# Performance work log

Measured on AMD Instinct MI355X. Metric: run time of the kernel, lower is better.

The kernel has to match this reference:

```python
import jax, jax.numpy as jnp
import numpy as np

DIM = 1024
HEADS = 16
HEAD_DIM = DIM // HEADS


def apply_rope(x):
    # x: (B, S, H, D)
    B, S, H, D = x.shape
    half = D // 2
    freqs = 1.0 / (10000.0 ** (jnp.arange(half, dtype=jnp.float32) / half))
    pos = jnp.arange(S, dtype=jnp.float32)
    angles = pos[:, None] * freqs[None, :]          # (S, half)
    sin = jnp.sin(angles)[None, :, None, :]
    cos = jnp.cos(angles)[None, :, None, :]
    x1, x2 = x[..., :half], x[..., half:]
    return jnp.concatenate([x1 * cos - x2 * sin, x1 * sin + x2 * cos], axis=-1)


def setup_inputs() -> dict:
    key = jax.random.key(0)
    ks = jax.random.split(key, 5)
    x = jax.random.normal(ks[0], (2, 2048, DIM), dtype=jnp.float32)
    s = 1.0 / np.sqrt(DIM)
    qkv_w = jax.random.uniform(ks[1], (3 * DIM, DIM), minval=-s, maxval=s, dtype=jnp.float32)
    qkv_b = jax.random.uniform(ks[2], (3 * DIM,), minval=-s, maxval=s, dtype=jnp.float32)
    proj_w = jax.random.uniform(ks[3], (DIM, DIM), minval=-s, maxval=s, dtype=jnp.float32)
    proj_b = jax.random.uniform(ks[4], (DIM,), minval=-s, maxval=s, dtype=jnp.float32)
    return {"x": x, "qkv_w": qkv_w, "qkv_b": qkv_b, "proj_w": proj_w, "proj_b": proj_b}


def reference(x, qkv_w, qkv_b, proj_w, proj_b):
    B, S, D = x.shape
    qkv = x @ qkv_w.T + qkv_b                       # (B, S, 3D)
    q, k, v = jnp.split(qkv, 3, axis=-1)
    q = q.reshape(B, S, HEADS, HEAD_DIM)
    k = k.reshape(B, S, HEADS, HEAD_DIM)
    v = v.reshape(B, S, HEADS, HEAD_DIM)
    q = apply_rope(q)
    k = apply_rope(k)
    scale = 1.0 / np.sqrt(HEAD_DIM)
    attn = jnp.einsum('bqhd,bkhd->bhqk', q, k) * scale
    mask = jnp.triu(jnp.ones((S, S), dtype=bool), k=1)
    attn = jnp.where(mask[None, None], -1e9, attn)
    attn = jax.nn.softmax(attn, axis=-1)
    out = jnp.einsum('bhqk,bkhd->bqhd', attn, v).reshape(B, S, D)
    return out @ proj_w.T + proj_b
```

## Files before the change

### kernel.cpp

```cpp
#include <hip/hip_runtime.h>
#include <hip/hip_bf16.h>
#include <stdint.h>

typedef unsigned short u16;
typedef __attribute__((ext_vector_type(8))) short bf16x8;
typedef __attribute__((ext_vector_type(4))) float f32x4;
typedef __attribute__((ext_vector_type(16))) float f32x16;

typedef __attribute__((address_space(1))) const void gas_t;
typedef __attribute__((address_space(3))) void las_t;

#define DEV __device__ __forceinline__

DEV float bf2f(u16 v){ union{uint32_t u; float f;} x; x.u = ((uint32_t)v)<<16; return x.f; }
DEV u16 f2bf(float f){ union{float f; uint32_t u;} x; x.f=f; uint32_t r = x.u + 0x7fff + ((x.u>>16)&1u); return (u16)(r>>16); }

DEV uint32_t pk2(float a, float b){
  return (uint32_t)f2bf(a) | ((uint32_t)f2bf(b)<<16);
}

DEV uint32_t cvtpk(float a, float b){
  uint32_t r;
  asm("v_cvt_pk_bf16_f32 %0, %1, %2" : "=v"(r) : "v"(a), "v"(b));
  return r;
}

DEV void xswap(uint32_t a, uint32_t b, int hi, uint32_t& ra, uint32_t& rb){
#if __has_builtin(__builtin_amdgcn_permlane32_swap)
  auto r = __builtin_amdgcn_permlane32_swap((int)a, (int)b, false, false);
  ra = (uint32_t)r[0]; rb = (uint32_t)r[1];
#else
  uint32_t sa = (uint32_t)__shfl_xor((int)a, 32);
  uint32_t sb = (uint32_t)__shfl_xor((int)b, 32);
  ra = hi ? sb : a;
  rb = hi ? b  : sa;
#endif
}

DEV void gload_lds16(const u16* g, u16* l){
  __builtin_amdgcn_global_load_lds((gas_t*)g, (las_t*)l, 16, 0, 0);
}

__global__ void cvt_f32_bf16(const float* __restrict__ src, u16* __restrict__ dst, int n4){
  int i = blockIdx.x*blockDim.x + threadIdx.x;
  if(i < n4){
    float4 v = ((const float4*)src)[i];
    ushort4 o; o.x=f2bf(v.x); o.y=f2bf(v.y); o.z=f2bf(v.z); o.w=f2bf(v.w);
    ((ushort4*)dst)[i] = o;
  }
}

template<int OUT_F32>
__global__ __launch_bounds__(256,3)
void gemm_bt(const u16* __restrict__ A, const u16* __restrict__ Bw,
             const float* __restrict__ bias, void* __restrict__ Cp, int N)
{
  constexpr int BK = 32, KSTEPS = 1024/BK;
  __shared__ __align__(16) u16 As[3][128][BK];
  __shared__ __align__(16) u16 Bs[3][128][BK];
  const int tid = threadIdx.x, w = tid>>6, l = tid&63;
  const int a = l&15, g = l>>4;
  const int m0 = blockIdx.y*128, n0 = blockIdx.x*128;
  const int wr = w>>1, wc = w&1;
  f32x4 zero = {0.f,0.f,0.f,0.f};
  f32x4 acc[4][4];
  #pragma unroll
  for(int m=0;m<4;m++) for(int n=0;n<4;n++) acc[m][n]=zero;

  const int srow = l>>2, scol = (l&3)*8;
  const u16* Ag = A  + (size_t)(m0 + w*32 + srow)*1024 + scol;
  const u16* Bg = Bw + (size_t)(n0 + w*32 + srow)*1024 + scol;

#define STAGE(KIDX, BUF) {                                        \
    u16* ab = &As[BUF][w*32][0];                                  \
    u16* bb = &Bs[BUF][w*32][0];                                  \
    gload_lds16(Ag + (KIDX)*BK,           ab);                    \
    gload_lds16(Ag + (KIDX)*BK + 16*1024, ab + 16*BK);            \
    gload_lds16(Bg + (KIDX)*BK,           bb);                    \
    gload_lds16(Bg + (KIDX)*BK + 16*1024, bb + 16*BK);            \
  }

  STAGE(0, 0);
  STAGE(1, 1);

  int bc = 0, bn = 2;
  for(int kt=0; kt<KSTEPS; ++kt){
    if(kt+1 < KSTEPS) asm volatile("s_waitcnt vmcnt(4)" ::: "memory");
    else              asm volatile("s_waitcnt vmcnt(0)" ::: "memory");
    __builtin_amdgcn_s_barrier();
    __builtin_amdgcn_sched_barrier(0);

    if(kt+2 < KSTEPS) STAGE(kt+2, bn);

    const u16* AsB = &As[bc][0][0];
    const u16* BsB = &Bs[bc][0][0];
    bf16x8 af[4], bf[4];
    #pragma unroll
    for(int m=0;m<4;m++) af[m] = *(const bf16x8*)(AsB + (wr*64 + m*16 + a)*BK + g*8);
    #pragma unroll
    for(int n=0;n<4;n++) bf[n] = *(const bf16x8*)(BsB + (wc*64 + n*16 + a)*BK + g*8);
    #pragma unroll
    for(int m=0;m<4;m++)
      #pragma unroll
      for(int n=0;n<4;n++)
        acc[m][n] = __builtin_amdgcn_mfma_f32_16x16x32_bf16(af[m], bf[n], acc[m][n], 0,0,0);

    bc = (bc==2) ? 0 : bc+1;
    bn = (bn==2) ? 0 : bn+1;
  }
#undef STAGE

  #pragma unroll
  for(int n=0;n<4;n++){
    int col = n0 + wc*64 + n*16 + a;
    float bv = bias[col];
    #pragma unroll
    for(int m=0;m<4;m++){
      int row = m0 + wr*64 + m*16 + g*4;
      #pragma unroll
      for(int r=0;r<4;r++){
        float v = acc[m][n][r] + bv;
        if(OUT_F32) ((float*)Cp)[(size_t)(row+r)*N + col] = v;
        else        ((u16*)Cp)[(size_t)(row+r)*N + col] = f2bf(v);
      }
    }
  }
}

__global__ void rope_relayout(const u16* __restrict__ qkv, u16* __restrict__ q_r,
                              u16* __restrict__ k_r)
{
  int t = blockIdx.x*256 + threadIdx.x;
  int gI = t&3, h=(t>>2)&15, row=t>>6;
  int s = row & 2047, b = row >> 11;
  int d0 = gI*8;
  const float QSC = 0.18033688011112042f;
  const u16* base = qkv + (size_t)row*3072 + h*64 + d0;
  union U { uint4 v; u16 e[8]; };
  U q1,q2,k1,k2, oq1,oq2,ok1,ok2;
  q1.v = *(const uint4*)(base);
  q2.v = *(const uint4*)(base+32);
  k1.v = *(const uint4*)(base+1024);
  k2.v = *(const uint4*)(base+1024+32);
  #pragma unroll
  for(int j=0;j<8;j++){
    float d = (float)(d0+j);
    float fr = __expf(-0.28782313662425574f * d);
    float ang = (float)s * fr;
    float sn, cs; sincosf(ang, &sn, &cs);
    float snq = sn*QSC, csq = cs*QSC;
    float x1 = bf2f(q1.e[j]), x2 = bf2f(q2.e[j]);
    oq1.e[j] = f2bf(x1*csq - x2*snq); oq2.e[j] = f2bf(x1*snq + x2*csq);
    x1 = bf2f(k1.e[j]); x2 = bf2f(k2.e[j]);
    ok1.e[j] = f2bf(x1*cs - x2*sn); ok2.e[j] = f2bf(x1*sn + x2*cs);
  }
  size_t o = ((size_t)(b*16+h)*2048 + s)*64 + d0;
  *(uint4*)(q_r+o) = oq1.v; *(uint4*)(q_r+o+32) = oq2.v;
  *(uint4*)(k_r+o) = ok1.v; *(uint4*)(k_r+o+32) = ok2.v;
}

__global__ __launch_bounds__(256,2)
void v_transpose(const u16* __restrict__ qkv, u16* __restrict__ vt)
{
  __shared__ uint32_t L[64*65];
  const int tid = threadIdx.x;
  const int bh = blockIdx.x & 31;
  const int stile = blockIdx.x >> 5;
  const int b = bh >> 4, h = bh & 15;
  const int s0 = stile*128;
  const int cg = tid & 7, sr = tid >> 3;
  const u16* src = qkv + (size_t)(b*2048 + s0)*3072 + 2048 + h*64 + cg*8;
  #pragma unroll
  for(int p=0;p<2;p++){
    int srow = p*64 + sr*2;
    union{uint4 v; u16 e[8];} v0, v1;
    v0.v = *(const uint4*)(src + (size_t)srow*3072);
    v1.v = *(const uint4*)(src + (size_t)(srow+1)*3072);
    #pragma unroll
    for(int jj=0;jj<8;jj++)
      L[(cg*8+jj)*65 + p*32 + sr] = (uint32_t)v0.e[jj] | ((uint32_t)v1.e[jj]<<16);
  }
  __syncthreads();
  const int w = tid>>6, ln = tid&63;
  u16* dst = vt + (size_t)bh*64*2048 + s0;
  #pragma unroll
  for(int dd=0;dd<16;dd++){
    int d = w*16 + dd;
    *(uint32_t*)(dst + (size_t)d*2048 + ln*2) = L[d*65 + ln];
  }
}

__global__ __launch_bounds__(256,4)
void attn_fwd8(const u16* __restrict__ Q, const u16* __restrict__ K,
               const u16* __restrict__ VT, u16* __restrict__ O)
{
  __shared__ __align__(16) u16 Ks[2][64][64];
  __shared__ __align__(16) u16 Vs[2][64][64];
  const int tid = threadIdx.x, w = tid>>6, ln = tid&63;
  const int lo = ln&31, hi = ln>>5;
  const int wq = w>>1, wk = w&1;
  const int b0 = blockIdx.x;
  const int bh = b0 & 31;
  const int j64 = 31 - (b0 >> 5);
  const int q0 = j64*64 + wq*32;
  const int nt = j64 + 1;

  const u16* Qb = Q  + ((size_t)bh*2048 + q0)*64;
  const u16* Kb = K  + (size_t)bh*2048*64;
  const u16* Vt = VT + (size_t)bh*64*2048;

  bf16x8 qf[4];
  #pragma unroll
  for(int s=0;s<4;s++) qf[s] = *(const bf16x8*)(Qb + lo*64 + s*16 + hi*8);

  const int rsub = ln>>3;
  const int coloff = ((ln&7) ^ rsub) * 8;
  const int wrow = (w&1)*32;
  const size_t rstride = (w<2) ? 64 : 2048;
  const u16* src0 = (w<2) ? (Kb + (size_t)(wrow+rsub)*64 + coloff)
                          : (Vt + (size_t)(wrow+rsub)*2048 + coloff);
  u16* ldsw = (w<2) ? (&Ks[0][0][0] + wrow*64) : (&Vs[0][0][0] + wrow*64);

  f32x16 oacc0, oacc1, z16;
  #pragma unroll
  for(int r=0;r<16;r++){ oacc0[r]=0.f; oacc1[r]=0.f; z16[r]=0.f; }
  float l_loc = 0.f;
  const int swz = (lo&7)<<4;

  #pragma unroll
  for(int g=0;g<4;g++) gload_lds16(src0 + (size_t)g*8*rstride, ldsw + g*512);
  __syncthreads();

  int buf = 0;
  for(int t=0; t<nt; ++t){
    if(t+1 < nt){
      const size_t koff = (w<2) ? (size_t)(t+1)*64*64 : (size_t)(t+1)*64;
      u16* dst = ldsw + (buf^1)*4096;
      #pragma unroll
      for(int g=0;g<4;g++) gload_lds16(src0 + koff + (size_t)g*8*rstride, dst + g*512);
    }

    const int kv32 = t*64 + wk*32;
    if(kv32 <= q0 + 31){
      const u16* KsB = &Ks[buf][0][0];
      const u16* VsB = &Vs[buf][0][0];
      bf16x8 kf[4], vf[4];
      #pragma unroll
      for(int s=0;s<4;s++)
        kf[s] = *(const bf16x8*)(KsB + (wk*32+lo)*64 + (((s*32 + hi*16) ^ swz)>>1));
      #pragma unroll
      for(int dt=0;dt<2;dt++)
        #pragma unroll
        for(int s2=0;s2<2;s2++)
          vf[dt*2+s2] = *(const bf16x8*)(VsB + (dt*32+lo)*64 + (((wk*64 + s2*32 + hi*16) ^ swz)>>1));

      f32x16 st = __builtin_amdgcn_mfma_f32_32x32x16_bf16(kf[0], qf[0], z16, 0,0,0);
      #pragma unroll
      for(int s=1;s<4;s++)
        st = __builtin_amdgcn_mfma_f32_32x32x16_bf16(kf[s], qf[s], st, 0,0,0);

      float p[16];
      #pragma unroll
      for(int r=0;r<16;r++) p[r] = exp2f(st[r]);
      if(kv32 == q0){
        #pragma unroll
        for(int r=0;r<16;r++){
          const int kvg = (r&3) + 8*(r>>2) + 4*hi;
          p[r] = (kvg <= lo) ? p[r] : 0.f;
        }
      }

      float sm[8];
      #pragma unroll
      for(int i=0;i<8;i++) sm[i] = p[i] + p[i+8];
      #pragma unroll
      for(int s=4;s>=1;s>>=1)
        #pragma unroll
        for(int i=0;i<s;i++) sm[i] += sm[i+s];
      l_loc += sm[0];

      uint32_t pk[8];
      #pragma unroll
      for(int i=0;i<8;i++) pk[i] = cvtpk(p[2*i], p[2*i+1]);

      union PF { bf16x8 v; uint32_t u[4]; } pf0, pf1;
      xswap(pk[0], pk[2], hi, pf0.u[0], pf0.u[2]);
      xswap(pk[1], pk[3], hi, pf0.u[1], pf0.u[3]);
      xswap(pk[4], pk[6], hi, pf1.u[0], pf1.u[2]);
      xswap(pk[5], pk[7], hi, pf1.u[1], pf1.u[3]);

      oacc0 = __builtin_amdgcn_mfma_f32_32x32x16_bf16(vf[0], pf0.v, oacc0, 0,0,0);
      oacc0 = __builtin_amdgcn_mfma_f32_32x32x16_bf16(vf[1], pf1.v, oacc0, 0,0,0);
      oacc1 = __builtin_amdgcn_mfma_f32_32x32x16_bf16(vf[2], pf0.v, oacc1, 0,0,0);
      oacc1 = __builtin_amdgcn_mfma_f32_32x32x16_bf16(vf[3], pf1.v, oacc1, 0,0,0);
    }
    __syncthreads();
    buf ^= 1;
  }

  float l_run = l_loc + __shfl_xor(l_loc, 32);

  float* LoC = (float*)&Ks[0][0][0];
  float* LlC = (float*)&Vs[0][0][0];
  if(wk == 1){
    #pragma unroll
    for(int r=0;r<16;r++){
      const int d = 4*hi + (r&3) + 8*(r>>2);
      LoC[(wq*64 + d   )*32 + lo] = oacc0[r];
      LoC[(wq*64 + d+32)*32 + lo] = oacc1[r];
    }
    if(hi==0) LlC[wq*32 + lo] = l_run;
  }
  __syncthreads();
  if(wk == 0){
    l_run += LlC[wq*32 + lo];
    #pragma unroll
    for(int r=0;r<16;r++){
      const int d = 4*hi + (r&3) + 8*(r>>2);
      oacc0[r] += LoC[(wq*64 + d   )*32 + lo];
      oacc1[r] += LoC[(wq*64 + d+32)*32 + lo];
    }
    const float invl = 1.f / l_run;
    const int row_g = (bh>>4)*2048 + q0 + lo;
    u16* Ob = O + (size_t)row_g*1024 + (bh&15)*64;
    #pragma unroll
    for(int g2=0; g2<4; g2++){
      uint2 pr;
      pr.x = pk2(oacc0[4*g2+0]*invl, oacc0[4*g2+1]*invl);
      pr.y = pk2(oacc0[4*g2+2]*invl, oacc0[4*g2+3]*invl);
      *(uint2*)(Ob + 8*g2 + 4*hi) = pr;
    }
    #pragma unroll
    for(int g2=0; g2<4; g2++){
      uint2 pr;
      pr.x = pk2(oacc1[4*g2+0]*invl, oacc1[4*g2+1]*invl);
      pr.y = pk2(oacc1[4*g2+2]*invl, oacc1[4*g2+3]*invl);
      *(uint2*)(Ob + 32 + 8*g2 + 4*hi) = pr;
    }
  }
}

extern "C" void kernel_launch(void* const* d_in, const int* in_sizes, int n_in,
                              void* d_out, int out_size, void* d_ws, size_t ws_size,
                              hipStream_t stream)
{
  const float* x      = (const float*)d_in[0];
  const float* qkv_w  = (const float*)d_in[1];
  const float* qkv_b  = (const float*)d_in[2];
  const float* proj_w = (const float*)d_in[3];
  const float* proj_b = (const float*)d_in[4];
  float* out = (float*)d_out;
  char* ws = (char*)d_ws;

  u16* xb    = (u16*)(ws);
  u16* wqkv  = (u16*)(ws + 8388608);
  u16* wproj = (u16*)(ws + 8388608 + 6291456);
  u16* qkvr  = (u16*)(ws + 16777216);
  u16* q_r   = (u16*)(ws + 41943040);
  u16* k_r   = q_r + 4194304;
  u16* vt    = k_r + 4194304;
  u16* o_b   = xb;

  cvt_f32_bf16<<<4096,256,0,stream>>>(x, xb, 1048576);
  cvt_f32_bf16<<<3072,256,0,stream>>>(qkv_w, wqkv, 786432);
  cvt_f32_bf16<<<1024,256,0,stream>>>(proj_w, wproj, 262144);

  dim3 gA(24,32);
  gemm_bt<0><<<gA,256,0,stream>>>(xb, wqkv, qkv_b, qkvr, 3072);

  rope_relayout<<<1024,256,0,stream>>>(qkvr, q_r, k_r);
  v_transpose<<<512,256,0,stream>>>(qkvr, vt);

  attn_fwd8<<<1024,256,0,stream>>>(q_r, k_r, vt, o_b);

  dim3 gC(8,32);
  gemm_bt<1><<<gC,256,0,stream>>>(o_b, wproj, proj_b, out, 1024);
}
```

Baseline: 120.7 us.

## Fuse rope and V transpose, swizzle QKV GEMM blocks, stage bf16 epilogue via LDS

Merges the rope relayout and V-transpose kernels into one launch, which removes a kernel launch and shares the block's (b,h,s) tiling. The QKV GEMM now runs on a 1D grid remapped into 8x8 supertiles for better L2 reuse of A and B tiles. Its bf16 epilogue writes through LDS so each row is stored with coalesced 16-byte writes instead of scattered 2-byte stores. The cost is an extra barrier and LDS round-trip in the epilogue, plus more work per block in the fused kernel.

```diff
diff --git a/kernel.cpp b/kernel.cpp
--- a/kernel.cpp
+++ b/kernel.cpp
@@ -50,17 +50,25 @@
   }
 }
 
-template<int OUT_F32>
+template<int OUT_F32, int SWZ>
 __global__ __launch_bounds__(256,3)
 void gemm_bt(const u16* __restrict__ A, const u16* __restrict__ Bw,
              const float* __restrict__ bias, void* __restrict__ Cp, int N)
 {
   constexpr int BK = 32, KSTEPS = 1024/BK;
-  __shared__ __align__(16) u16 As[3][128][BK];
-  __shared__ __align__(16) u16 Bs[3][128][BK];
+  __shared__ __align__(16) u16 pool[3*8192];
   const int tid = threadIdx.x, w = tid>>6, l = tid&63;
   const int a = l&15, g = l>>4;
-  const int m0 = blockIdx.y*128, n0 = blockIdx.x*128;
+  int bx, by;
+  if(SWZ){
+    const int bid = blockIdx.x;
+    const int st = bid >> 6, q = bid & 63;
+    bx = (st % 3)*8 + (q & 7);
+    by = (st / 3)*8 + (q >> 3);
+  } else {
+    bx = blockIdx.x; by = blockIdx.y;
+  }
+  const int m0 = by*128, n0 = bx*128;
   const int wr = w>>1, wc = w&1;
   f32x4 zero = {0.f,0.f,0.f,0.f};
   f32x4 acc[4][4];
@@ -72,12 +80,12 @@
   const u16* Bg = Bw + (size_t)(n0 + w*32 + srow)*1024 + scol;
 
 #define STAGE(KIDX, BUF) {                                        \
-    u16* ab = &As[BUF][w*32][0];                                  \
-    u16* bb = &Bs[BUF][w*32][0];                                  \
+    u16* ab = pool + (BUF)*8192 + w*1024;                         \
+    u16* bb = pool + (BUF)*8192 + 4096 + w*1024;                  \
     gload_lds16(Ag + (KIDX)*BK,           ab);                    \
-    gload_lds16(Ag + (KIDX)*BK + 16*1024, ab + 16*BK);            \
+    gload_lds16(Ag + (KIDX)*BK + 16*1024, ab + 512);              \
     gload_lds16(Bg + (KIDX)*BK,           bb);                    \
-    gload_lds16(Bg + (KIDX)*BK + 16*1024, bb + 16*BK);            \
+    gload_lds16(Bg + (KIDX)*BK + 16*1024, bb + 512);              \
   }
 
   STAGE(0, 0);
@@ -92,8 +100,8 @@
 
     if(kt+2 < KSTEPS) STAGE(kt+2, bn);
 
-    const u16* AsB = &As[bc][0][0];
-    const u16* BsB = &Bs[bc][0][0];
+    const u16* AsB = pool + bc*8192;
+    const u16* BsB = AsB + 4096;
     bf16x8 af[4], bf[4];
     #pragma unroll
     for(int m=0;m<4;m++) af[m] = *(const bf16x8*)(AsB + (wr*64 + m*16 + a)*BK + g*8);
@@ -110,57 +118,44 @@
   }
 #undef STAGE
 
-  #pragma unroll
-  for(int n=0;n<4;n++){
-    int col = n0 + wc*64 + n*16 + a;
-    float bv = bias[col];
-    #pragma unroll
-    for(int m=0;m<4;m++){
-      int row = m0 + wr*64 + m*16 + g*4;
-      #pragma unroll
-      for(int r=0;r<4;r++){
-        float v = acc[m][n][r] + bv;
-        if(OUT_F32) ((float*)Cp)[(size_t)(row+r)*N + col] = v;
-        else        ((u16*)Cp)[(size_t)(row+r)*N + col] = f2bf(v);
+  if(OUT_F32){
+    #pragma unroll
+    for(int n=0;n<4;n++){
+      int col = n0 + wc*64 + n*16 + a;
+      float bv = bias[col];
+      #pragma unroll
+      for(int m=0;m<4;m++){
+        int row = m0 + wr*64 + m*16 + g*4;
+        #pragma unroll
+        for(int r=0;r<4;r++)
+          ((float*)Cp)[(size_t)(row+r)*N + col] = acc[m][n][r] + bv;
       }
     }
-  }
-}
-
-__global__ void rope_relayout(const u16* __restrict__ qkv, u16* __restrict__ q_r,
-                              u16* __restrict__ k_r)
-{
-  int t = blockIdx.x*256 + threadIdx.x;
-  int gI = t&3, h=(t>>2)&15, row=t>>6;
-  int s = row & 2047, b = row >> 11;
-  int d0 = gI*8;
-  const float QSC = 0.18033688011112042f;
-  const u16* base = qkv + (size_t)row*3072 + h*64 + d0;
-  union U { uint4 v; u16 e[8]; };
-  U q1,q2,k1,k2, oq1,oq2,ok1,ok2;
-  q1.v = *(const uint4*)(base);
-  q2.v = *(const uint4*)(base+32);
-  k1.v = *(const uint4*)(base+1024);
-  k2.v = *(const uint4*)(base+1024+32);
-  #pragma unroll
-  for(int j=0;j<8;j++){
-    float d = (float)(d0+j);
-    float fr = __expf(-0.28782313662425574f * d);
-    float ang = (float)s * fr;
-    float sn, cs; sincosf(ang, &sn, &cs);
-    float snq = sn*QSC, csq = cs*QSC;
-    float x1 = bf2f(q1.e[j]), x2 = bf2f(q2.e[j]);
-    oq1.e[j] = f2bf(x1*csq - x2*snq); oq2.e[j] = f2bf(x1*snq + x2*csq);
-    x1 = bf2f(k1.e[j]); x2 = bf2f(k2.e[j]);
-    ok1.e[j] = f2bf(x1*cs - x2*sn); ok2.e[j] = f2bf(x1*sn + x2*cs);
-  }
-  size_t o = ((size_t)(b*16+h)*2048 + s)*64 + d0;
-  *(uint4*)(q_r+o) = oq1.v; *(uint4*)(q_r+o+32) = oq2.v;
-  *(uint4*)(k_r+o) = ok1.v; *(uint4*)(k_r+o+32) = ok2.v;
+  } else {
+    __syncthreads();
+    u16* cw = pool + (size_t)w*4608;
+    #pragma unroll
+    for(int n=0;n<4;n++){
+      float bv = bias[n0 + wc*64 + n*16 + a];
+      #pragma unroll
+      for(int m=0;m<4;m++)
+        #pragma unroll
+        for(int r=0;r<4;r++)
+          cw[(m*16 + g*4 + r)*72 + n*16 + a] = f2bf(acc[m][n][r] + bv);
+    }
+    u16* Cb = (u16*)Cp + (size_t)(m0 + wr*64)*N + n0 + wc*64;
+    #pragma unroll
+    for(int rr=0;rr<8;rr++){
+      int row = rr*8 + (l>>3);
+      uint4 v = *(const uint4*)(cw + row*72 + (l&7)*8);
+      *(uint4*)(Cb + (size_t)row*N + (l&7)*8) = v;
+    }
+  }
 }
 
 __global__ __launch_bounds__(256,2)
-void v_transpose(const u16* __restrict__ qkv, u16* __restrict__ vt)
+void rope_vt(const u16* __restrict__ qkv, u16* __restrict__ q_r,
+             u16* __restrict__ k_r, u16* __restrict__ vt)
 {
   __shared__ uint32_t L[64*65];
   const int tid = threadIdx.x;
@@ -168,25 +163,60 @@
   const int stile = blockIdx.x >> 5;
   const int b = bh >> 4, h = bh & 15;
   const int s0 = stile*128;
+
   const int cg = tid & 7, sr = tid >> 3;
-  const u16* src = qkv + (size_t)(b*2048 + s0)*3072 + 2048 + h*64 + cg*8;
-  #pragma unroll
-  for(int p=0;p<2;p++){
-    int srow = p*64 + sr*2;
-    union{uint4 v; u16 e[8];} v0, v1;
-    v0.v = *(const uint4*)(src + (size_t)srow*3072);
-    v1.v = *(const uint4*)(src + (size_t)(srow+1)*3072);
-    #pragma unroll
-    for(int jj=0;jj<8;jj++)
-      L[(cg*8+jj)*65 + p*32 + sr] = (uint32_t)v0.e[jj] | ((uint32_t)v1.e[jj]<<16);
+  const u16* vsrc = qkv + (size_t)(b*2048 + s0)*3072 + 2048 + h*64 + cg*8;
+  union U4 { uint4 v; u16 e[8]; };
+  U4 v0a, v1a, v0b, v1b;
+  v0a.v = *(const uint4*)(vsrc + (size_t)(sr*2    )*3072);
+  v1a.v = *(const uint4*)(vsrc + (size_t)(sr*2 + 1)*3072);
+  v0b.v = *(const uint4*)(vsrc + (size_t)(64 + sr*2    )*3072);
+  v1b.v = *(const uint4*)(vsrc + (size_t)(64 + sr*2 + 1)*3072);
+  #pragma unroll
+  for(int jj=0;jj<8;jj++){
+    L[(cg*8+jj)*65 + sr]      = (uint32_t)v0a.e[jj] | ((uint32_t)v1a.e[jj]<<16);
+    L[(cg*8+jj)*65 + 32 + sr] = (uint32_t)v0b.e[jj] | ((uint32_t)v1b.e[jj]<<16);
   }
   __syncthreads();
-  const int w = tid>>6, ln = tid&63;
-  u16* dst = vt + (size_t)bh*64*2048 + s0;
-  #pragma unroll
-  for(int dd=0;dd<16;dd++){
-    int d = w*16 + dd;
-    *(uint32_t*)(dst + (size_t)d*2048 + ln*2) = L[d*65 + ln];
+  {
+    const int w = tid>>6, ln = tid&63;
+    u16* dst = vt + (size_t)bh*64*2048 + s0;
+    #pragma unroll
+    for(int dd=0;dd<16;dd++){
+      int d = w*16 + dd;
+      *(uint32_t*)(dst + (size_t)d*2048 + ln*2) = L[d*65 + ln];
+    }
+  }
+
+  const float QSC = 0.18033688011112042f;
+  #pragma unroll
+  for(int it=0; it<2; ++it){
+    int t2 = it*256 + tid;
+    int row = t2>>2, gI = t2&3;
+    int s = s0 + row;
+    int d0 = gI*8;
+    const u16* base = qkv + (size_t)(b*2048 + s)*3072 + h*64 + d0;
+    union U { uint4 v; u16 e[8]; };
+    U q1,q2,k1,k2, oq1,oq2,ok1,ok2;
+    q1.v = *(const uint4*)(base);
+    q2.v = *(const uint4*)(base+32);
+    k1.v = *(const uint4*)(base+1024);
+    k2.v = *(const uint4*)(base+1024+32);
+    #pragma unroll
+    for(int j=0;j<8;j++){
+      float d = (float)(d0+j);
+      float fr = __expf(-0.28782313662425574f * d);
+      float ang = (float)s * fr;
+      float sn, cs; sincosf(ang, &sn, &cs);
+      float snq = sn*QSC, csq = cs*QSC;
+      float x1 = bf2f(q1.e[j]), x2 = bf2f(q2.e[j]);
+      oq1.e[j] = f2bf(x1*csq - x2*snq); oq2.e[j] = f2bf(x1*snq + x2*csq);
+      x1 = bf2f(k1.e[j]); x2 = bf2f(k2.e[j]);
+      ok1.e[j] = f2bf(x1*cs - x2*sn); ok2.e[j] = f2bf(x1*sn + x2*cs);
+    }
+    size_t o = ((size_t)bh*2048 + s)*64 + d0;
+    *(uint4*)(q_r+o) = oq1.v; *(uint4*)(q_r+o+32) = oq2.v;
+    *(uint4*)(k_r+o) = ok1.v; *(uint4*)(k_r+o+32) = ok2.v;
   }
 }
 
@@ -365,14 +395,12 @@
   cvt_f32_bf16<<<3072,256,0,stream>>>(qkv_w, wqkv, 786432);
   cvt_f32_bf16<<<1024,256,0,stream>>>(proj_w, wproj, 262144);
 
-  dim3 gA(24,32);
-  gemm_bt<0><<<gA,256,0,stream>>>(xb, wqkv, qkv_b, qkvr, 3072);
-
-  rope_relayout<<<1024,256,0,stream>>>(qkvr, q_r, k_r);
-  v_transpose<<<512,256,0,stream>>>(qkvr, vt);
+  gemm_bt<0,1><<<768,256,0,stream>>>(xb, wqkv, qkv_b, qkvr, 3072);
+
+  rope_vt<<<512,256,0,stream>>>(qkvr, q_r, k_r, vt);
 
   attn_fwd8<<<1024,256,0,stream>>>(q_r, k_r, vt, o_b);
 
   dim3 gC(8,32);
-  gemm_bt<1><<<gC,256,0,stream>>>(o_b, wproj, proj_b, out, 1024);
-}
+  gemm_bt<1,0><<<gC,256,0,stream>>>(o_b, wproj, proj_b, out, 1024);
+}
```

Result: faster. 109.8 us (-9.0%).
